# Kernel optimization log

Measured on AMD Instinct MI355X. Metric: run time of the kernel, lower is better.

## Reference

```python
import jax, jax.numpy as jnp
import numpy as np

BETA = 0.9
ADAPT_RATE = 0.1


def _surrogate_spike(x):
    gate = jax.nn.sigmoid(5.0 * x)
    hard = (x > 0).astype(x.dtype)
    return jax.lax.stop_gradient(hard - gate) + gate


def setup_inputs() -> dict:
    key = jax.random.key(0)
    k1, k2, k3, k4, k5 = jax.random.split(key, 5)
    B, T, D, H = 64, 256, 512, 1024
    x = jax.random.normal(k1, (B, T, D), dtype=jnp.float32)
    # fc_in: Linear(D, H); fc_out: Linear(H, 1)
    W_in = jax.random.normal(k2, (H, D), dtype=jnp.float32) * (1.0 / np.sqrt(D))
    b_in = jax.random.normal(k3, (H,), dtype=jnp.float32) * 0.01
    W_out = jax.random.normal(k4, (1, H), dtype=jnp.float32) * (1.0 / np.sqrt(H))
    b_out = jax.random.normal(k5, (1,), dtype=jnp.float32) * 0.01
    return {"x": x, "W_in": W_in, "b_in": b_in, "W_out": W_out, "b_out": b_out}


def reference(x, W_in, b_in, W_out, b_out):
    B, T, D = x.shape
    H = W_in.shape[0]
    # batch fc_in over all timesteps outside the recurrence
    pre = jnp.einsum('btd,hd->bth', x, W_in) + b_in  # [B,T,H]

    def step(carry, p_t):
        mem, adapt = carry
        mem = BETA * mem + p_t - adapt
        spk = _surrogate_spike(mem)
        adapt = adapt + ADAPT_RATE * spk
        mem = mem - spk  # reset_mode == 'subtract'
        return (mem, adapt), spk

    init = (jnp.zeros((B, H), x.dtype), jnp.zeros((B, H), x.dtype))
    _, spks = jax.lax.scan(step, init, jnp.swapaxes(pre, 0, 1))  # spks: [T,B,H]

    # mean_t fc_out(spk_t) == fc_out(mean_t spk_t) since fc_out is affine
    spk_mean = spks.mean(axis=0)  # [B,H]
    return spk_mean @ W_out.T + b_out  # [B,1]
```

## Files before the change

### kernel.cpp

```cpp
#include <hip/hip_runtime.h>

constexpr int Bb = 64;
constexpr int Tt = 256;
constexpr int Dd = 512;
constexpr int Hh = 1024;
constexpr int Mm = Bb * Tt;

typedef _Float16 half8 __attribute__((ext_vector_type(8)));
typedef _Float16 half4v __attribute__((ext_vector_type(4)));
typedef float floatx16 __attribute__((ext_vector_type(16)));

#define GPTR(x) ((const __attribute__((address_space(1))) void*)(x))
#define LPTR(x) ((__attribute__((address_space(3))) void*)(x))

__global__ __launch_bounds__(256) void convert_t(const float* __restrict__ x,
                                                 const float* __restrict__ Win,
                                                 _Float16* __restrict__ xh,
                                                 _Float16* __restrict__ xl,
                                                 _Float16* __restrict__ wh,
                                                 _Float16* __restrict__ wl,
                                                 const float* __restrict__ bout,
                                                 float* __restrict__ out) {
    __shared__ _Float16 lh[64 * 72];
    __shared__ _Float16 ll[64 * 72];
    const int tid = threadIdx.x;
    const int k0 = blockIdx.x * 64;

    if (blockIdx.x == 0 && blockIdx.y == 0 && tid < Bb) out[tid] = bout[0];

    const float* src;
    _Float16 *dh, *dl;
    int nrows, m0;
    if (blockIdx.y < 256) {
        src = x; dh = xh; dl = xl; nrows = Mm; m0 = blockIdx.y * 64;
    } else {
        src = Win; dh = wh; dl = wl; nrows = Hh; m0 = (blockIdx.y - 256) * 64;
    }

#pragma unroll
    for (int i = 0; i < 4; ++i) {
        const int lin = tid + i * 256;
        const int row = lin >> 4;
        const int c4 = (lin & 15) * 4;
        const float4 v = *(const float4*)(src + (size_t)(m0 + row) * Dd + k0 + c4);
        const float va[4] = {v.x, v.y, v.z, v.w};
        half4v h, l;
#pragma unroll
        for (int q = 0; q < 4; ++q) {
            const _Float16 hi = (_Float16)va[q];
            h[q] = hi;
            l[q] = (_Float16)((va[q] - (float)hi) * 4096.0f);
        }
        *(half4v*)&lh[row * 72 + c4] = h;
        *(half4v*)&ll[row * 72 + c4] = l;
    }
    __syncthreads();
#pragma unroll
    for (int i = 0; i < 2; ++i) {
        const int lin = tid + i * 256;
        const int kc = lin >> 6;
        const int mm = lin & 63;
        const half8 h = *(const half8*)&lh[mm * 72 + kc * 8];
        const half8 l = *(const half8*)&ll[mm * 72 + kc * 8];
        const size_t g = (size_t)(k0 / 8 + kc) * nrows + m0 + mm;
        *(half8*)(dh + g * 8) = h;
        *(half8*)(dl + g * 8) = l;
    }
}

__global__ __launch_bounds__(256) void gemm_f16x2(const _Float16* __restrict__ xh,
                                                  const _Float16* __restrict__ xl,
                                                  const _Float16* __restrict__ wh,
                                                  const _Float16* __restrict__ wl,
                                                  const float* __restrict__ bin,
                                                  float* __restrict__ pre) {
    __shared__ _Float16 lds[2][2][4096];

    const int tid = threadIdx.x;
    const int id = blockIdx.x;
    const int j  = id & 7;
    const int s  = id >> 3;
    const int m0 = (((s >> 3) << 3) | j) * 128;
    const int n0 = (s & 7) * 128;

    const int lane = tid & 63;
    const int wave = tid >> 6;
    const int wm = (wave & 1) * 64;
    const int wn = (wave >> 1) * 64;
    const int lr = lane & 31;
    const int lk = lane >> 5;

    floatx16 acc[2][2], accx[2][2];
#pragma unroll
    for (int mi = 0; mi < 2; ++mi)
#pragma unroll
        for (int ni = 0; ni < 2; ++ni)
#pragma unroll
            for (int r = 0; r < 16; ++r) { acc[mi][ni][r] = 0.0f; accx[mi][ni][r] = 0.0f; }

#define STAGE_A(buf, kc0)                                                            \
    do {                                                                             \
        _Pragma("unroll")                                                            \
        for (int i_ = 0; i_ < 2; ++i_) {                                             \
            const int c_ = tid + i_ * 256;                                           \
            const int kp_ = c_ >> 7;                                                 \
            const int row_ = c_ & 127;                                               \
            const size_t ga_ = ((size_t)((kc0) + kp_) * Mm + m0 + row_) * 8;         \
            __builtin_amdgcn_global_load_lds(GPTR(xh + ga_), LPTR(&lds[buf][0][c_ * 8]), 16, 0, 0); \
            __builtin_amdgcn_global_load_lds(GPTR(xl + ga_), LPTR(&lds[buf][1][c_ * 8]), 16, 0, 0); \
        }                                                                            \
    } while (0)

    const size_t bbase = (size_t)(n0 + wn + lr) * 8;
    half8 bset[2][4];
#define LOAD_B(rot, hs)                                                              \
    do {                                                                             \
        const size_t off_ = (size_t)((hs) * 2 + lk) * (Hh * 8) + bbase;              \
        bset[rot][0] = *(const half8*)(wh + off_);                                   \
        bset[rot][1] = *(const half8*)(wh + off_ + 256);                             \
        bset[rot][2] = *(const half8*)(wl + off_);                                   \
        bset[rot][3] = *(const half8*)(wl + off_ + 256);                             \
    } while (0)

    STAGE_A(0, 0);
    LOAD_B(0, 0);

    for (int ss = 0; ss < 16; ++ss) {
        __syncthreads();
        if (ss < 15) STAGE_A((ss + 1) & 1, (ss + 1) * 4);
        const int cur = ss & 1;
#pragma unroll
        for (int s2 = 0; s2 < 2; ++s2) {
            const int hs = ss * 2 + s2;
            const int rot = hs & 1;
            if (hs < 31) LOAD_B(rot ^ 1, hs + 1);

            half8 ah[2], al[2];
#pragma unroll
            for (int mi = 0; mi < 2; ++mi) {
                const int ci = (s2 * 2 + lk) * 128 + wm + mi * 32 + lr;
                ah[mi] = *(const half8*)&lds[cur][0][ci * 8];
                al[mi] = *(const half8*)&lds[cur][1][ci * 8];
            }
#pragma unroll
            for (int mi = 0; mi < 2; ++mi)
#pragma unroll
                for (int ni = 0; ni < 2; ++ni) {
                    acc[mi][ni]  = __builtin_amdgcn_mfma_f32_32x32x16_f16(ah[mi], bset[rot][ni],     acc[mi][ni], 0, 0, 0);
                    accx[mi][ni] = __builtin_amdgcn_mfma_f32_32x32x16_f16(ah[mi], bset[rot][2 + ni], accx[mi][ni], 0, 0, 0);
                    accx[mi][ni] = __builtin_amdgcn_mfma_f32_32x32x16_f16(al[mi], bset[rot][ni],     accx[mi][ni], 0, 0, 0);
                }
        }
    }
#undef STAGE_A
#undef LOAD_B

    const float bv0 = bin[n0 + wn + lr];
    const float bv1 = bin[n0 + wn + 32 + lr];
#pragma unroll
    for (int mi = 0; mi < 2; ++mi)
#pragma unroll
        for (int ni = 0; ni < 2; ++ni) {
            const float bv = ni ? bv1 : bv0;
#pragma unroll
            for (int r = 0; r < 16; ++r) {
                const int row = (r & 3) + 8 * (r >> 2) + 4 * lk;
                const int m = m0 + wm + mi * 32 + row;
                const int n = n0 + wn + ni * 32 + lr;
                pre[(size_t)m * Hh + n] =
                    acc[mi][ni][r] + accx[mi][ni][r] * (1.0f / 4096.0f) + bv;
            }
        }
}

#define BK 16
#define BMP 132
__global__ __launch_bounds__(256) void gemm_pre(const float* __restrict__ x,
                                                const float* __restrict__ Win,
                                                const float* __restrict__ bin,
                                                float* __restrict__ pre) {
    __shared__ float As[BK][BMP];
    __shared__ float Bs[BK][BMP];
    const int tid = threadIdx.x;
    const int m0 = blockIdx.y * 128;
    const int n0 = blockIdx.x * 128;
    const int tx = tid & 15;
    const int ty = tid >> 4;
    float acc[8][8];
#pragma unroll
    for (int i = 0; i < 8; ++i)
#pragma unroll
        for (int jj = 0; jj < 8; ++jj) acc[i][jj] = 0.0f;
    const float* Aptr = x + (size_t)m0 * Dd;
    const float* Bptr = Win + (size_t)n0 * Dd;
    for (int k0 = 0; k0 < Dd; k0 += BK) {
#pragma unroll
        for (int i = 0; i < 2; ++i) {
            const int lin = tid + i * 256;
            const int row = lin >> 2;
            const int kq = (lin & 3) << 2;
            const float4 av = *(const float4*)(Aptr + (size_t)row * Dd + k0 + kq);
            const float4 bv = *(const float4*)(Bptr + (size_t)row * Dd + k0 + kq);
            As[kq + 0][row] = av.x; As[kq + 1][row] = av.y;
            As[kq + 2][row] = av.z; As[kq + 3][row] = av.w;
            Bs[kq + 0][row] = bv.x; Bs[kq + 1][row] = bv.y;
            Bs[kq + 2][row] = bv.z; Bs[kq + 3][row] = bv.w;
        }
        __syncthreads();
#pragma unroll
        for (int kk = 0; kk < BK; ++kk) {
            const float4 a0 = *(const float4*)&As[kk][ty * 4];
            const float4 a1 = *(const float4*)&As[kk][ty * 4 + 64];
            const float4 b0 = *(const float4*)&Bs[kk][tx * 4];
            const float4 b1 = *(const float4*)&Bs[kk][tx * 4 + 64];
            const float a[8] = {a0.x, a0.y, a0.z, a0.w, a1.x, a1.y, a1.z, a1.w};
            const float b[8] = {b0.x, b0.y, b0.z, b0.w, b1.x, b1.y, b1.z, b1.w};
#pragma unroll
            for (int i = 0; i < 8; ++i)
#pragma unroll
                for (int jj = 0; jj < 8; ++jj) acc[i][jj] += a[i] * b[jj];
        }
        __syncthreads();
    }
#pragma unroll
    for (int i = 0; i < 8; ++i) {
        const int m = m0 + ((i < 4) ? (ty * 4 + i) : (64 + ty * 4 + i - 4));
#pragma unroll
        for (int half = 0; half < 2; ++half) {
            const int n = n0 + tx * 4 + half * 64;
            float4 v;
            v.x = acc[i][half * 4 + 0] + bin[n + 0];
            v.y = acc[i][half * 4 + 1] + bin[n + 1];
            v.z = acc[i][half * 4 + 2] + bin[n + 2];
            v.w = acc[i][half * 4 + 3] + bin[n + 3];
            *(float4*)(pre + (size_t)m * Hh + n) = v;
        }
    }
}

__global__ __launch_bounds__(64) void init_out(const float* __restrict__ bout,
                                               float* __restrict__ out) {
    out[threadIdx.x] = bout[0];
}

__global__ __launch_bounds__(64) void alif_scan(const float* __restrict__ pre,
                                                const float* __restrict__ Wout,
                                                float* __restrict__ out) {
    const int h = blockIdx.x * 64 + threadIdx.x;
    const int b = blockIdx.y;
    const float* p = pre + (size_t)b * Tt * Hh + h;

    float buf[32];
#pragma unroll
    for (int jj = 0; jj < 32; ++jj) buf[jj] = p[(size_t)jj * Hh];

    float mem = 0.0f, adapt = 0.0f, cnt = 0.0f;
    for (int t0 = 0; t0 < Tt; t0 += 32) {
        float cur[32];
#pragma unroll
        for (int jj = 0; jj < 32; ++jj) cur[jj] = buf[jj];
        if (t0 + 32 < Tt) {
#pragma unroll
            for (int jj = 0; jj < 32; ++jj) buf[jj] = p[(size_t)(t0 + 32 + jj) * Hh];
        }
#pragma unroll
        for (int jj = 0; jj < 32; ++jj) {
            mem = 0.9f * mem + cur[jj] - adapt;
            const float spk = (mem > 0.0f) ? 1.0f : 0.0f;
            adapt += 0.1f * spk;
            mem -= spk;
            cnt += spk;
        }
    }

    float val = cnt * Wout[h] * (1.0f / (float)Tt);
#pragma unroll
    for (int off = 32; off > 0; off >>= 1) val += __shfl_down(val, off, 64);
    if (threadIdx.x == 0) atomicAdd(&out[b], val);
}

extern "C" void kernel_launch(void* const* d_in, const int* in_sizes, int n_in,
                              void* d_out, int out_size, void* d_ws, size_t ws_size,
                              hipStream_t stream) {
    const float* x    = (const float*)d_in[0];
    const float* Win  = (const float*)d_in[1];
    const float* bin  = (const float*)d_in[2];
    const float* Wout = (const float*)d_in[3];
    const float* bout = (const float*)d_in[4];
    float* out = (float*)d_out;

    const size_t pre_bytes = (size_t)Mm * Hh * 4;
    const size_t xh_bytes  = (size_t)Mm * Dd * 2;
    const size_t wh_bytes  = (size_t)Hh * Dd * 2;
    float* pre = (float*)d_ws;

    const size_t need = pre_bytes + 2 * xh_bytes + 2 * wh_bytes + 4096;
    if (ws_size >= need) {
        char* base = (char*)d_ws + pre_bytes;
        _Float16* xh = (_Float16*)base;
        _Float16* xl = (_Float16*)(base + xh_bytes);
        _Float16* wh = (_Float16*)(base + 2 * xh_bytes);
        _Float16* wl = (_Float16*)(base + 2 * xh_bytes + wh_bytes);

        convert_t<<<dim3(8, 272), 256, 0, stream>>>(x, Win, xh, xl, wh, wl, bout, out);

        gemm_f16x2<<<1024, 256, 0, stream>>>(xh, xl, wh, wl, bin, pre);

        alif_scan<<<dim3(Hh / 64, Bb), 64, 0, stream>>>(pre, Wout, out);
    } else {
        init_out<<<1, 64, 0, stream>>>(bout, out);
        dim3 g1(Hh / 128, Mm / 128);
        gemm_pre<<<g1, 256, 0, stream>>>(x, Win, bin, pre);
        alif_scan<<<dim3(Hh / 64, Bb), 64, 0, stream>>>(pre, Wout, out);
    }
}
```

Baseline: 152.6 us.

## Fuse spiking scan into split-f16 GEMM epilogue, eliminate pre buffer

The GEMM is retiled so each block covers all 256 timesteps of one batch row and 64 hidden units. The adaptive LIF recurrence then runs in the epilogue from LDS instead of writing the 64 MB fp32 pre tensor and re-reading it in a separate scan kernel. This removes a large global write and read plus one launch. The cost is a serial 256-step scan run by only 32 threads per 32-column half, with the rest of the block idle, and a different tile shape for the MFMA main loop.

```diff
diff --git a/kernel.cpp b/kernel.cpp
--- a/kernel.cpp
+++ b/kernel.cpp
@@ -68,25 +68,26 @@
     }
 }
 
-__global__ __launch_bounds__(256) void gemm_f16x2(const _Float16* __restrict__ xh,
-                                                  const _Float16* __restrict__ xl,
-                                                  const _Float16* __restrict__ wh,
-                                                  const _Float16* __restrict__ wl,
-                                                  const float* __restrict__ bin,
-                                                  float* __restrict__ pre) {
-    __shared__ _Float16 lds[2][2][4096];
+__global__ __launch_bounds__(256, 2) void gemm_fused(const _Float16* __restrict__ xh,
+                                                     const _Float16* __restrict__ xl,
+                                                     const _Float16* __restrict__ wh,
+                                                     const _Float16* __restrict__ wl,
+                                                     const float* __restrict__ bin,
+                                                     const float* __restrict__ Wout,
+                                                     float* __restrict__ out) {
+    __shared__ _Float16 ldsA[2][2][8192];
 
     const int tid = threadIdx.x;
     const int id = blockIdx.x;
     const int j  = id & 7;
-    const int s  = id >> 3;
-    const int m0 = (((s >> 3) << 3) | j) * 128;
-    const int n0 = (s & 7) * 128;
+    const int q  = id >> 3;
+    const int nt = q & 15;
+    const int b  = (q >> 4) * 8 + j;
+    const int m0 = b * Tt;
+    const int n0 = nt * 64;
 
     const int lane = tid & 63;
     const int wave = tid >> 6;
-    const int wm = (wave & 1) * 64;
-    const int wn = (wave >> 1) * 64;
     const int lr = lane & 31;
     const int lk = lane >> 5;
 
@@ -101,17 +102,17 @@
 #define STAGE_A(buf, kc0)                                                            \
     do {                                                                             \
         _Pragma("unroll")                                                            \
-        for (int i_ = 0; i_ < 2; ++i_) {                                             \
+        for (int i_ = 0; i_ < 4; ++i_) {                                             \
             const int c_ = tid + i_ * 256;                                           \
-            const int kp_ = c_ >> 7;                                                 \
-            const int row_ = c_ & 127;                                               \
+            const int kp_ = c_ >> 8;                                                 \
+            const int row_ = c_ & 255;                                               \
             const size_t ga_ = ((size_t)((kc0) + kp_) * Mm + m0 + row_) * 8;         \
-            __builtin_amdgcn_global_load_lds(GPTR(xh + ga_), LPTR(&lds[buf][0][c_ * 8]), 16, 0, 0); \
-            __builtin_amdgcn_global_load_lds(GPTR(xl + ga_), LPTR(&lds[buf][1][c_ * 8]), 16, 0, 0); \
+            __builtin_amdgcn_global_load_lds(GPTR(xh + ga_), LPTR(&ldsA[buf][0][c_ * 8]), 16, 0, 0); \
+            __builtin_amdgcn_global_load_lds(GPTR(xl + ga_), LPTR(&ldsA[buf][1][c_ * 8]), 16, 0, 0); \
         }                                                                            \
     } while (0)
 
-    const size_t bbase = (size_t)(n0 + wn + lr) * 8;
+    const size_t bbase = (size_t)(n0 + lr) * 8;
     half8 bset[2][4];
 #define LOAD_B(rot, hs)                                                              \
     do {                                                                             \
@@ -138,9 +139,9 @@
             half8 ah[2], al[2];
 #pragma unroll
             for (int mi = 0; mi < 2; ++mi) {
-                const int ci = (s2 * 2 + lk) * 128 + wm + mi * 32 + lr;
-                ah[mi] = *(const half8*)&lds[cur][0][ci * 8];
-                al[mi] = *(const half8*)&lds[cur][1][ci * 8];
+                const int ci = (s2 * 2 + lk) * 256 + wave * 64 + mi * 32 + lr;
+                ah[mi] = *(const half8*)&ldsA[cur][0][ci * 8];
+                al[mi] = *(const half8*)&ldsA[cur][1][ci * 8];
             }
 #pragma unroll
             for (int mi = 0; mi < 2; ++mi)
@@ -155,22 +156,45 @@
 #undef STAGE_A
 #undef LOAD_B
 
-    const float bv0 = bin[n0 + wn + lr];
-    const float bv1 = bin[n0 + wn + 32 + lr];
-#pragma unroll
-    for (int mi = 0; mi < 2; ++mi)
-#pragma unroll
-        for (int ni = 0; ni < 2; ++ni) {
-            const float bv = ni ? bv1 : bv0;
+    __syncthreads();
+    float* scanbuf = (float*)ldsA;
+
+    float bsum = 0.0f;
+#pragma unroll
+    for (int p = 0; p < 2; ++p) {
+        const float bv = bin[n0 + p * 32 + lr];
+#pragma unroll
+        for (int mi = 0; mi < 2; ++mi)
 #pragma unroll
             for (int r = 0; r < 16; ++r) {
                 const int row = (r & 3) + 8 * (r >> 2) + 4 * lk;
-                const int m = m0 + wm + mi * 32 + row;
-                const int n = n0 + wn + ni * 32 + lr;
-                pre[(size_t)m * Hh + n] =
-                    acc[mi][ni][r] + accx[mi][ni][r] * (1.0f / 4096.0f) + bv;
+                const int t = wave * 64 + mi * 32 + row;
+                scanbuf[t * 33 + lr] = acc[mi][p][r] + accx[mi][p][r] * (1.0f / 4096.0f) + bv;
             }
-        }
+        __syncthreads();
+
+        float val = 0.0f;
+        if (tid < 32) {
+            float mem = 0.0f, adapt = 0.0f, cnt = 0.0f;
+#pragma unroll 8
+            for (int t = 0; t < Tt; ++t) {
+                const float v = scanbuf[t * 33 + tid];
+                mem = 0.9f * mem + v - adapt;
+                const float spk = (mem > 0.0f) ? 1.0f : 0.0f;
+                adapt += 0.1f * spk;
+                mem -= spk;
+                cnt += spk;
+            }
+            val = cnt * Wout[n0 + p * 32 + tid] * (1.0f / (float)Tt);
+        }
+        if (tid < 64) {
+#pragma unroll
+            for (int off = 16; off > 0; off >>= 1) val += __shfl_down(val, off, 64);
+            if (tid == 0) bsum += val;
+        }
+        __syncthreads();
+    }
+    if (tid == 0) atomicAdd(&out[b], bsum);
 }
 
 #define BK 16
@@ -289,14 +313,12 @@
     const float* bout = (const float*)d_in[4];
     float* out = (float*)d_out;
 
-    const size_t pre_bytes = (size_t)Mm * Hh * 4;
-    const size_t xh_bytes  = (size_t)Mm * Dd * 2;
-    const size_t wh_bytes  = (size_t)Hh * Dd * 2;
-    float* pre = (float*)d_ws;
-
-    const size_t need = pre_bytes + 2 * xh_bytes + 2 * wh_bytes + 4096;
+    const size_t xh_bytes = (size_t)Mm * Dd * 2;
+    const size_t wh_bytes = (size_t)Hh * Dd * 2;
+    const size_t need = 2 * xh_bytes + 2 * wh_bytes + 4096;
+
     if (ws_size >= need) {
-        char* base = (char*)d_ws + pre_bytes;
+        char* base = (char*)d_ws;
         _Float16* xh = (_Float16*)base;
         _Float16* xl = (_Float16*)(base + xh_bytes);
         _Float16* wh = (_Float16*)(base + 2 * xh_bytes);
@@ -304,10 +326,9 @@
 
         convert_t<<<dim3(8, 272), 256, 0, stream>>>(x, Win, xh, xl, wh, wl, bout, out);
 
-        gemm_f16x2<<<1024, 256, 0, stream>>>(xh, xl, wh, wl, bin, pre);
-
-        alif_scan<<<dim3(Hh / 64, Bb), 64, 0, stream>>>(pre, Wout, out);
+        gemm_fused<<<1024, 256, 0, stream>>>(xh, xl, wh, wl, bin, Wout, out);
     } else {
+        float* pre = (float*)d_ws;
         init_out<<<1, 64, 0, stream>>>(bout, out);
         dim3 g1(Hh / 128, Mm / 128);
         gemm_pre<<<g1, 256, 0, stream>>>(x, Win, bin, pre);
```

New measurement: 161.7 us. 1.06x slower.
